# Performance work log

Measured on AMD Instinct MI355X. Metric: run time of the kernel, lower is better.

## Reference

```python
import jax, jax.numpy as jnp
import numpy as np
from jax import lax


def _connected_components(fg2d):
    """4-connected component labeling of a boolean mask via min-label
    propagation with pointer-jumping compression (union-find style).
    Returns flat int32 labels; each component is labeled by its minimum
    flat pixel index; background pixels get sentinel label N."""
    H, W = fg2d.shape
    N = H * W
    sent = jnp.array([N], jnp.int32)
    idx = jnp.arange(N, dtype=jnp.int32)
    lab0 = jnp.where(fg2d.reshape(-1), idx, jnp.int32(N))
    n_compress = int(np.ceil(np.log2(max(N, 2)))) + 1

    def nb_min(lab):
        l2 = lab.reshape(H, W)
        p = jnp.pad(l2, 1, constant_values=N)  # out-of-bounds -> sentinel
        m = jnp.minimum(jnp.minimum(p[:-2, 1:-1], p[2:, 1:-1]),
                        jnp.minimum(p[1:-1, :-2], p[1:-1, 2:]))
        m = jnp.minimum(l2, m)
        return jnp.where(fg2d, m, jnp.int32(N)).reshape(-1)

    def compress(_, lab):
        ext = jnp.concatenate([lab, sent])  # index N maps to sentinel
        return jnp.minimum(lab, ext[lab])

    def body(c):
        lab, _ = c
        new = nb_min(lab)
        new = lax.fori_loop(0, n_compress, compress, new)
        return (new, jnp.any(new != lab))

    lab, _ = lax.while_loop(lambda c: c[1], body, (lab0, jnp.bool_(True)))
    return lab


def setup_inputs() -> dict:
    key = jax.random.key(0)
    x = jax.random.normal(key, (1, 1536, 2048, 2), dtype=jnp.float32)
    return {"x": x}


def reference(x):
    H, W = x.shape[1], x.shape[2]
    N = H * W
    # threshold score maps
    textmap = jnp.where(x[0, :, :, 0] > 0.4, 1.0, 0.0)
    linkmap = jnp.where(x[0, :, :, 1] > 0.4, 1.0, 0.0)
    comb = jnp.clip(textmap + linkmap, 0.0, 1.0)
    # 3x3 grayscale dilation with a ones filter == 3x3 max-pool (+1 offset);
    # foreground for labeling is the binary dilation of the combined mask
    dil = lax.reduce_window(comb, jnp.float32(0.0), lax.max, (3, 3), (1, 1), 'SAME')
    fg2d = dil > 0.0
    seg = _connected_components(fg2d)  # [N], background -> segment N
    idx = jnp.arange(N, dtype=jnp.int32)
    rows = idx // W
    cols = idx % W
    ns = N + 1
    # per-component bbox via segment reductions (fused replacement for the
    # per-label full-image mask scans in the original)
    ymin = jax.ops.segment_min(rows, seg, num_segments=ns)[:N]
    ymax = jax.ops.segment_max(rows, seg, num_segments=ns)[:N]
    xmin = jax.ops.segment_min(cols, seg, num_segments=ns)[:N]
    xmax = jax.ops.segment_max(cols, seg, num_segments=ns)[:N]
    tmax = jax.ops.segment_max(textmap.reshape(-1), seg, num_segments=ns)[:N]
    count = jax.ops.segment_sum(jnp.ones((N,), jnp.int32), seg, num_segments=ns)[:N]
    h = ymax - ymin
    w = xmax - xmin
    valid = (count > 0) & (h > 4) & (w > 4) & (tmax > 0.7)
    bboxes = jnp.where(valid[:, None], jnp.stack([ymin, xmin, h, w], axis=-1), 0)
    return bboxes, valid
```

## Files before the change

### kernel.cpp

```cpp
#include <hip/hip_runtime.h>
#include <climits>
#include <stdint.h>

typedef unsigned int u32;
typedef unsigned long long u64;
typedef int v4i __attribute__((ext_vector_type(4)));

#define HH 1536
#define WW 2048
#define NPIX (HH*WW)
#define WSHIFT 11
#define WPR 64
#define SH 8
#define NS 192
#define RPR 32
#define SLOTS (SH*RPR)
#define NCAP 1024
#define BSLOT 8
#define NTH (NPIX/4)

#define GLD(p) __hip_atomic_load((p), __ATOMIC_RELAXED, __HIP_MEMORY_SCOPE_AGENT)

__global__ void k_flags(const float4* __restrict__ xv4,
                        u64* __restrict__ combp64, u64* __restrict__ textp64,
                        v4i* __restrict__ out4, int* __restrict__ ctrs) {
    int tid = blockIdx.x * 256 + threadIdx.x;
    int l = threadIdx.x & 63, wv = threadIdx.x >> 6;
    float4 a = xv4[tid * 2 + 0];
    float4 b = xv4[tid * 2 + 1];
    u32 nc = 0, nt = 0;
    { u32 tx = a.x > 0.4f, cb = tx | (a.y > 0.4f); nc |= cb;      nt |= tx; }
    { u32 tx = a.z > 0.4f, cb = tx | (a.w > 0.4f); nc |= cb << 1; nt |= tx << 1; }
    { u32 tx = b.x > 0.4f, cb = tx | (b.y > 0.4f); nc |= cb << 2; nt |= tx << 2; }
    { u32 tx = b.z > 0.4f, cb = tx | (b.w > 0.4f); nc |= cb << 3; nt |= tx << 3; }
    u64 vc = (u64)nc << (4 * (l & 15));
    u64 vt = (u64)nt << (4 * (l & 15));
    #pragma unroll
    for (int o = 1; o < 16; o <<= 1) {
        vc |= __shfl_xor(vc, o);
        vt |= __shfl_xor(vt, o);
    }
    if ((l & 15) == 0) {
        int w = blockIdx.x * 16 + wv * 4 + (l >> 4);
        combp64[w] = vc;
        textp64[w] = vt;
    }
    v4i z = {0, 0, 0, 0};
    #pragma unroll
    for (int k = 0; k < 5; ++k)
        out4[tid + k * NTH] = z;
    if (tid == 0) { ctrs[0] = 0; ctrs[1] = 0; }
}

__device__ __forceinline__ int lfind_h(int* L, int x) {
    while (true) {
        int p = L[x];
        if (p == x) return x;
        int g = L[p];
        if (g == p) return p;
        L[x] = g;
        x = g;
    }
}

__device__ __forceinline__ void lmerge(int* L, int a, int b) {
    while (true) {
        a = lfind_h(L, a);
        b = lfind_h(L, b);
        if (a == b) return;
        if (a < b) { int s = a; a = b; b = s; }
        int old = atomicMin(&L[a], b);
        if (old == a) return;
        a = old;
    }
}

__global__ __launch_bounds__(512) void k_stripf(
        const u32* __restrict__ combp, const u32* __restrict__ textp,
        u32* __restrict__ brun_se, int* __restrict__ brun_id,
        u64* __restrict__ bpack, int* __restrict__ bcnt,
        int* __restrict__ groots, int* __restrict__ ctrs,
        v4i* __restrict__ obb, int* __restrict__ oval) {
    __shared__ u32 sb[SH][RPR], eb[SH][RPR];
    __shared__ u32 rec[SLOTS];
    __shared__ int lab[SLOTS];
    __shared__ int a0[SLOTS], a1[SLOTS], a2[SLOTS], a3[SLOTS], atx[SLOTS];
    __shared__ int nodemap[SLOTS];
    __shared__ int nper[SH];
    __shared__ int wtot[8], woff[8];
    __shared__ int sBase, sLast;
    __shared__ u64 sbpk[NS * 2 * BSLOT];
    __shared__ int sbc[NS * 2];
    __shared__ int flab[NCAP];
    __shared__ int f0[NCAP], f1[NCAP], f2[NCAP], f3[NCAP], ftx2[NCAP], fpix[NCAP];

    int strip = blockIdx.x;
    int rbase = strip * SH;
    int t = threadIdx.x;
    int wv = t >> 6, l = t & 63;

    u32 tK;
    int nrW;
    {
        int lr = wv;
        int r = rbase + lr;
        int base = r * WPR + l;
        u32 c0 = combp[base];
        u32 cm = (r > 0)      ? combp[base - WPR] : 0u;
        u32 cp = (r < HH - 1) ? combp[base + WPR] : 0u;
        u32 v = c0 | cm | cp;
        u32 vl = __shfl_up(v, 1);   if (l == 0)  vl = 0;
        u32 vr = __shfl_down(v, 1); if (l == 63) vr = 0;
        u32 f = v | (v << 1) | (v >> 1) | (vl >> 31) | (vr << 31);
        u32 flw = __shfl_up(f, 1);   if (l == 0)  flw = 0;
        u32 frw = __shfl_down(f, 1); if (l == 63) frw = 0;
        u32 smask = f & ~((f << 1) | (flw >> 31));
        u32 emask = f & ~((f >> 1) | ((frw & 1u) << 31));
        int ns = __popc(smask), ne = __popc(emask);
        int is = ns, ie = ne;
        #pragma unroll
        for (int o = 1; o < 64; o <<= 1) {
            int a = __shfl_up(is, o); if (l >= o) is += a;
            int b = __shfl_up(ie, o); if (l >= o) ie += b;
        }
        int ks = is - ns, ke = ie - ne;
        u32 m = smask; int k = ks;
        while (m) { int b = __ffs(m) - 1; m &= m - 1; if (k < RPR) sb[lr][k] = (u32)(l * 32 + b); ++k; }
        m = emask; k = ke;
        while (m) { int b = __ffs(m) - 1; m &= m - 1; if (k < RPR) eb[lr][k] = (u32)(l * 32 + b); ++k; }
        nrW = min(__shfl(is, 63), RPR);
        tK = textp[base] & f;
        if (l == 0) nper[lr] = nrW;
    }
    if (t < SLOTS) {
        lab[t] = t; a0[t] = 0; a1[t] = 0; a2[t] = 0; a3[t] = 0; atx[t] = 0;
        nodemap[t] = -1;
    }
    __syncthreads();

    {
        int lr = wv;
        int nr = nrW;
        u32 txtm = 0;
        for (int kk = 0; kk < nr; ++kk) {
            int st = (int)sb[lr][kk], en = (int)eb[lr][kk];
            int lo = max(st - l * 32, 0), hi = min(en - l * 32, 31);
            u32 mask = 0;
            if (lo <= hi)
                mask = ((hi == 31) ? 0xFFFFFFFFu : ((1u << (hi + 1)) - 1u)) & ~((1u << lo) - 1u);
            int any = __any((tK & mask) != 0);
            txtm |= (any ? 1u : 0u) << kk;
        }
        if (l < nr)
            rec[lr * RPR + l] = sb[lr][l] | (eb[lr][l] << 11) | (((txtm >> l) & 1u) << 22);
    }
    __syncthreads();

    if (t < SH - 1) {
        int na = nper[t], nb = nper[t + 1];
        int i = 0, j = 0;
        while (i < na && j < nb) {
            u32 ra = rec[t * RPR + i], rb = rec[(t + 1) * RPR + j];
            int sa = ra & 2047, ea = (ra >> 11) & 2047;
            int sb2 = rb & 2047, eb2 = (rb >> 11) & 2047;
            if (sa <= eb2 && sb2 <= ea) lmerge(lab, t * RPR + i, (t + 1) * RPR + j);
            if (ea <= eb2) ++i; else ++j;
        }
    }
    __syncthreads();

    #pragma unroll
    for (int pass = 0; pass < 5; ++pass) {
        if (t < SLOTS) {
            int p = lab[t], g = lab[p];
            if (g != p) lab[t] = g;
        }
        __syncthreads();
    }

    int occ = (t < SLOTS) && ((t & (RPR - 1)) < nper[t >> 5]);
    if (occ) {
        u32 rc_ = rec[t];
        int st_ = rc_ & 2047, en_ = (rc_ >> 11) & 2047, tb = (int)((rc_ >> 22) & 1u);
        int r = rbase + (t >> 5);
        int root = lab[t];
        atomicMax(&a0[root], 2047 - r);
        atomicMax(&a1[root], r + 1);
        atomicMax(&a2[root], 2048 - st_);
        atomicMax(&a3[root], en_ + 1);
        if (tb) atomicOr(&atx[root], 1);
    }
    __syncthreads();

    int flag = occ && (lab[t] == t);
    u64 bmask = __ballot(flag);
    int lanepfx = __popcll(bmask & ((1ull << l) - 1ull));
    if (l == 0) wtot[wv] = __popcll(bmask);
    __syncthreads();
    if (t == 0) {
        int s = 0;
        for (int w2 = 0; w2 < 8; ++w2) { woff[w2] = s; s += wtot[w2]; }
        sBase = atomicAdd(&ctrs[1], s);
    }
    __syncthreads();
    if (flag) {
        int node = sBase + woff[wv] + lanepfx;
        if (node < NCAP) {
            nodemap[t] = node;
            int g = node * 8;
            int r = rbase + (t >> 5);
            groots[g + 0] = a0[t];
            groots[g + 1] = a1[t];
            groots[g + 2] = a2[t];
            groots[g + 3] = a3[t];
            groots[g + 4] = atx[t];
            groots[g + 5] = (r << WSHIFT) | (int)(rec[t] & 2047);
        }
    }
    __syncthreads();

    if (t < SLOTS) {
        int lr = t >> 5, k = t & (RPR - 1);
        if ((lr == 0 || lr == SH - 1) && k < nper[lr]) {
            int side = (lr == 0) ? 0 : 1;
            int id = nodemap[lab[t]];
            if (k < BSLOT)
                bpack[(strip * 2 + side) * BSLOT + k] =
                    (u64)rec[t] | ((u64)(u32)(id + 1) << 32);
            int o = (strip * 2 + side) * RPR + k;
            brun_se[o] = rec[t];
            brun_id[o] = id;
        }
    }
    if (t == 0) {
        bcnt[strip * 2 + 0] = nper[0];
        bcnt[strip * 2 + 1] = nper[SH - 1];
    }
    __syncthreads();

    if (t == 0) {
        __threadfence();
        int old = __hip_atomic_fetch_add(&ctrs[0], 1, __ATOMIC_ACQ_REL,
                                         __HIP_MEMORY_SCOPE_AGENT);
        sLast = (old == NS - 1);
    }
    __syncthreads();
    if (!sLast) return;

    int ncnt = min(ctrs[1], NCAP);
    for (int n = t; n < ncnt; n += 512) {
        flab[n] = n; f0[n] = 0; f1[n] = 0; f2[n] = 0; f3[n] = 0;
        ftx2[n] = 0; fpix[n] = INT_MAX;
    }
    for (int s = t; s < NS * 2; s += 512) sbc[s] = bcnt[s];
    #pragma unroll
    for (int u = t; u < NS * 2 * BSLOT; u += 512) sbpk[u] = bpack[u];
    __syncthreads();

    if (t < NS - 1) {
        int A = t * 2 + 1, B = (t + 1) * 2;
        int na = sbc[A], nb = sbc[B];
        if (na <= BSLOT && nb <= BSLOT) {
            int i = 0, j = 0;
            while (i < na && j < nb) {
                u64 pa = sbpk[A * BSLOT + i], pb = sbpk[B * BSLOT + j];
                u32 ra = (u32)pa, rb = (u32)pb;
                int sa = ra & 2047, ea = (ra >> 11) & 2047;
                int sb2 = rb & 2047, eb2 = (rb >> 11) & 2047;
                if (sa <= eb2 && sb2 <= ea) {
                    int ia = (int)(pa >> 32) - 1, ib = (int)(pb >> 32) - 1;
                    if (ia >= 0 && ib >= 0) lmerge(flab, ia, ib);
                }
                if (ea <= eb2) ++i; else ++j;
            }
        } else {
            int i = 0, j = 0;
            while (i < na && j < nb) {
                u32 ra = GLD(&brun_se[A * RPR + i]), rb = GLD(&brun_se[B * RPR + j]);
                int sa = ra & 2047, ea = (ra >> 11) & 2047;
                int sb2 = rb & 2047, eb2 = (rb >> 11) & 2047;
                if (sa <= eb2 && sb2 <= ea) {
                    int ia = GLD(&brun_id[A * RPR + i]), ib = GLD(&brun_id[B * RPR + j]);
                    if (ia >= 0 && ib >= 0) lmerge(flab, ia, ib);
                }
                if (ea <= eb2) ++i; else ++j;
            }
        }
    }
    __syncthreads();

    #pragma unroll
    for (int pass = 0; pass < 5; ++pass) {
        for (int n = t; n < ncnt; n += 512) {
            int p = flab[n], g = flab[p];
            if (g != p) flab[n] = g;
        }
        __syncthreads();
    }

    for (int n = t; n < ncnt; n += 512) {
        int R = flab[n];
        v4i lo = *(const v4i*)&groots[n * 8];
        v4i hi = *(const v4i*)&groots[n * 8 + 4];
        atomicMax(&f0[R], lo.x);
        atomicMax(&f1[R], lo.y);
        atomicMax(&f2[R], lo.z);
        atomicMax(&f3[R], lo.w);
        if (hi.x) atomicOr(&ftx2[R], 1);
        atomicMin(&fpix[R], hi.y);
    }
    __syncthreads();

    for (int n = t; n < ncnt; n += 512) {
        if (flab[n] == n) {
            int ym = 2047 - f0[n], yx = f1[n] - 1;
            int xm = 2048 - f2[n], xx = f3[n] - 1;
            int h = yx - ym, w = xx - xm;
            if (h > 4 && w > 4 && ftx2[n]) {
                int p = fpix[n];
                v4i bb = {ym, xm, h, w};
                obb[p] = bb;
                oval[p] = 1;
            }
        }
    }
}

extern "C" void kernel_launch(void* const* d_in, const int* in_sizes, int n_in,
                              void* d_out, int out_size, void* d_ws, size_t ws_size,
                              hipStream_t stream) {
    const float* x = (const float*)d_in[0];

    u32* combp   = (u32*)d_ws;
    u32* textp   = combp + NPIX / 32;
    int* groots  = (int*)(textp + NPIX / 32);
    u64* bpack   = (u64*)(groots + NCAP * 8);
    u32* brun_se = (u32*)(bpack + NS * 2 * BSLOT);
    int* brun_id = (int*)(brun_se + NS * 2 * RPR);
    int* bcnt    = brun_id + NS * 2 * RPR;
    int* ctrs    = bcnt + NS * 2;

    int* obb  = (int*)d_out;
    int* oval = obb + (size_t)NPIX * 4;

    k_flags<<<NPIX / 4 / 256, 256, 0, stream>>>((const float4*)x, (u64*)combp,
                                                (u64*)textp, (v4i*)d_out, ctrs);
    k_stripf<<<NS, 512, 0, stream>>>(combp, textp, brun_se, brun_id, bpack,
                                     bcnt, groots, ctrs, (v4i*)obb, oval);
}
```

Measured before the change: 108.1 us.

## Move output zeroing into strip kernel and use 256 six-row strips

Zeroing of the bbox and valid output buffers moves out of the thresholding kernel and into the strip labeling kernel. Each strip block clears its own slice before doing its labeling work, and it does this before the fence and completion counter, so the last block's writes still land after all the zeros. Strip height drops from 8 to 6 rows, giving 256 blocks of 384 threads instead of 192 blocks of 512, which is meant to spread the work over more compute units. The final pointer-jumping pass count rises by one to cover the extra cross-strip merges, and each block now carries a larger share of the memory-write traffic.

```diff
diff --git a/kernel.cpp b/kernel.cpp
--- a/kernel.cpp
+++ b/kernel.cpp
@@ -11,19 +11,22 @@
 #define NPIX (HH*WW)
 #define WSHIFT 11
 #define WPR 64
-#define SH 8
-#define NS 192
+#define SH 6
+#define NS 256
+#define TPB (SH*64)
 #define RPR 32
 #define SLOTS (SH*RPR)
 #define NCAP 1024
 #define BSLOT 8
-#define NTH (NPIX/4)
+#define NZV4 (NPIX*5/4)
+#define ZPB (NZV4/NS)
+#define ZIT (ZPB/TPB)
 
 #define GLD(p) __hip_atomic_load((p), __ATOMIC_RELAXED, __HIP_MEMORY_SCOPE_AGENT)
 
 __global__ void k_flags(const float4* __restrict__ xv4,
                         u64* __restrict__ combp64, u64* __restrict__ textp64,
-                        v4i* __restrict__ out4, int* __restrict__ ctrs) {
+                        int* __restrict__ ctrs) {
     int tid = blockIdx.x * 256 + threadIdx.x;
     int l = threadIdx.x & 63, wv = threadIdx.x >> 6;
     float4 a = xv4[tid * 2 + 0];
@@ -45,10 +48,6 @@
         combp64[w] = vc;
         textp64[w] = vt;
     }
-    v4i z = {0, 0, 0, 0};
-    #pragma unroll
-    for (int k = 0; k < 5; ++k)
-        out4[tid + k * NTH] = z;
     if (tid == 0) { ctrs[0] = 0; ctrs[1] = 0; }
 }
 
@@ -75,7 +74,7 @@
     }
 }
 
-__global__ __launch_bounds__(512) void k_stripf(
+__global__ __launch_bounds__(TPB) void k_stripf(
         const u32* __restrict__ combp, const u32* __restrict__ textp,
         u32* __restrict__ brun_se, int* __restrict__ brun_id,
         u64* __restrict__ bpack, int* __restrict__ bcnt,
@@ -87,7 +86,7 @@
     __shared__ int a0[SLOTS], a1[SLOTS], a2[SLOTS], a3[SLOTS], atx[SLOTS];
     __shared__ int nodemap[SLOTS];
     __shared__ int nper[SH];
-    __shared__ int wtot[8], woff[8];
+    __shared__ int wtot[SH], woff[SH];
     __shared__ int sBase, sLast;
     __shared__ u64 sbpk[NS * 2 * BSLOT];
     __shared__ int sbc[NS * 2];
@@ -98,6 +97,14 @@
     int rbase = strip * SH;
     int t = threadIdx.x;
     int wv = t >> 6, l = t & 63;
+
+    {
+        v4i z = {0, 0, 0, 0};
+        v4i* oz = obb + (size_t)strip * ZPB;
+        #pragma unroll
+        for (int k = 0; k < ZIT; ++k)
+            oz[k * TPB + t] = z;
+    }
 
     u32 tK;
     int nrW;
@@ -199,7 +206,7 @@
     __syncthreads();
     if (t == 0) {
         int s = 0;
-        for (int w2 = 0; w2 < 8; ++w2) { woff[w2] = s; s += wtot[w2]; }
+        for (int w2 = 0; w2 < SH; ++w2) { woff[w2] = s; s += wtot[w2]; }
         sBase = atomicAdd(&ctrs[1], s);
     }
     __syncthreads();
@@ -248,13 +255,12 @@
     if (!sLast) return;
 
     int ncnt = min(ctrs[1], NCAP);
-    for (int n = t; n < ncnt; n += 512) {
+    for (int n = t; n < ncnt; n += TPB) {
         flab[n] = n; f0[n] = 0; f1[n] = 0; f2[n] = 0; f3[n] = 0;
         ftx2[n] = 0; fpix[n] = INT_MAX;
     }
-    for (int s = t; s < NS * 2; s += 512) sbc[s] = bcnt[s];
-    #pragma unroll
-    for (int u = t; u < NS * 2 * BSLOT; u += 512) sbpk[u] = bpack[u];
+    for (int s = t; s < NS * 2; s += TPB) sbc[s] = bcnt[s];
+    for (int u = t; u < NS * 2 * BSLOT; u += TPB) sbpk[u] = bpack[u];
     __syncthreads();
 
     if (t < NS - 1) {
@@ -290,15 +296,15 @@
     __syncthreads();
 
     #pragma unroll
-    for (int pass = 0; pass < 5; ++pass) {
-        for (int n = t; n < ncnt; n += 512) {
+    for (int pass = 0; pass < 6; ++pass) {
+        for (int n = t; n < ncnt; n += TPB) {
             int p = flab[n], g = flab[p];
             if (g != p) flab[n] = g;
         }
         __syncthreads();
     }
 
-    for (int n = t; n < ncnt; n += 512) {
+    for (int n = t; n < ncnt; n += TPB) {
         int R = flab[n];
         v4i lo = *(const v4i*)&groots[n * 8];
         v4i hi = *(const v4i*)&groots[n * 8 + 4];
@@ -311,7 +317,7 @@
     }
     __syncthreads();
 
-    for (int n = t; n < ncnt; n += 512) {
+    for (int n = t; n < ncnt; n += TPB) {
         if (flab[n] == n) {
             int ym = 2047 - f0[n], yx = f1[n] - 1;
             int xm = 2048 - f2[n], xx = f3[n] - 1;
@@ -344,7 +350,7 @@
     int* oval = obb + (size_t)NPIX * 4;
 
     k_flags<<<NPIX / 4 / 256, 256, 0, stream>>>((const float4*)x, (u64*)combp,
-                                                (u64*)textp, (v4i*)d_out, ctrs);
-    k_stripf<<<NS, 512, 0, stream>>>(combp, textp, brun_se, brun_id, bpack,
+                                                (u64*)textp, ctrs);
+    k_stripf<<<NS, TPB, 0, stream>>>(combp, textp, brun_se, brun_id, bpack,
                                      bcnt, groots, ctrs, (v4i*)obb, oval);
 }
```

New measurement: 110.2 us. +2.0%, slower.
